# Kernel tuning notes

Hardware: AMD Instinct MI355X
Metric: run time of the kernel (lower is better)

The kernel has to match this reference:

```python
import jax, jax.numpy as jnp
import numpy as np

B, LQ, LK, D = 8, 1024, 4096, 1024


def setup_inputs() -> dict:
    key = jax.random.key(0)
    k1, k2, k3, k4, k5, k6 = jax.random.split(key, 6)
    s = 1.0 / np.sqrt(D)
    return {
        "T": jax.random.normal(k1, (B, LQ, D), dtype=jnp.float32),
        "S": jax.random.normal(k2, (B, LK, D), dtype=jnp.float32),
        "Wq": jax.random.uniform(k3, (D, D), jnp.float32, -s, s),
        "Wk": jax.random.uniform(k4, (D, D), jnp.float32, -s, s),
        "Wv": jax.random.uniform(k5, (D, D), jnp.float32, -s, s),
        "Wo": jax.random.uniform(k6, (D, D), jnp.float32, -s, s),
    }


def reference(T, S, Wq, Wk, Wv, Wo):
    # Linear layers: y = x @ W.T (torch nn.Linear convention), bias=False
    q = jnp.einsum('bqd,ed->bqe', T, Wq)          # [B, LQ, D]
    k = jnp.einsum('bkd,ed->bke', S, Wk)          # [B, LK, D]
    v = jnp.einsum('bkd,ed->bke', S, Wv)          # [B, LK, D]
    scale = jnp.asarray(D, q.dtype) ** -0.5        # hidden_dim ** -0.5 (single head)
    attn = jnp.einsum('bqe,bke->bqk', q, k) * scale  # [B, LQ, LK]
    attn = jax.nn.softmax(attn, axis=-1)
    out = jnp.einsum('bqk,bke->bqe', attn, v)      # [B, LQ, D]
    return jnp.einsum('bqe,fe->bqf', out, Wo)      # output projection
```

## Files before the change

### kernel.cpp

```cpp
#include <hip/hip_runtime.h>
#include <stdint.h>

typedef __bf16 bf16;
typedef __bf16 bf16x8 __attribute__((ext_vector_type(8)));
typedef float f32x4 __attribute__((ext_vector_type(4)));

__device__ __forceinline__ void gload_lds16(const void* g, void* l) {
    __builtin_amdgcn_global_load_lds(
        (const __attribute__((address_space(1))) unsigned int*)g,
        (__attribute__((address_space(3))) unsigned int*)l, 16, 0, 0);
}

#define BAR()    asm volatile("s_barrier" ::: "memory")
#define WAITV(N) asm volatile("s_waitcnt vmcnt(" #N ")" ::: "memory")

template<int OMODE>
__global__ __launch_bounds__(512, 2)
void gemm256(const bf16* __restrict__ A, const bf16* __restrict__ B,
             void* __restrict__ Cv, int K, int N,
             long batchA, long batchB, long batchC, float alpha,
             int nbx, int nby, int GC)
{
    __shared__ __align__(16) bf16 lds[2][4][8192];

    const int nwg  = gridDim.x;
    const int orig = blockIdx.x;
    const int q8   = nwg >> 3, r8 = nwg & 7;
    const int xcd  = orig & 7, lid = orig >> 3;
    const int p    = (xcd < r8 ? xcd * (q8 + 1) : r8 * (q8 + 1) + (xcd - r8) * q8) + lid;
    const int perb = nbx * nby;
    const int z    = p / perb;
    const int pb   = p - z * perb;
    const int sw   = nby * GC;
    const int st   = pb / sw;
    const int rem  = pb - st * sw;
    const int by   = rem / GC;
    const int bx   = st * GC + (rem - by * GC);

    const long rowb = (long)by << 8;
    const long colb = (long)bx << 8;

    const int t  = threadIdx.x;
    const int l  = t & 63;
    const int w  = t >> 6;
    const int wm = w >> 2;
    const int wn = w & 3;

    const int sL   = (t * 16) ^ (((t >> 3) & 3) << 4);
    const int srow = sL >> 6;
    const int sk   = (sL & 63) >> 1;
    const bf16* Ab = A + (long)z * batchA;
    const bf16* Bb = B + (long)z * batchB;
    const bf16* gA = Ab + (rowb + srow) * (long)K + sk;
    const bf16* gB = Bb + (colb + srow) * (long)K + sk;
    const long rstep = 128L * K;
    const int  d0 = t * 8, d1 = t * 8 + 4096;

    const int xl    = ((l >> 1) & 3) << 4;
    const int aBase = ((wm * 128 + (l & 15)) * 64 + ((l >> 4) << 4)) ^ xl;
    const int bBase = ((wn * 64  + (l & 15)) * 64 + ((l >> 4) << 4)) ^ xl;

    f32x4 acc[8][4] = {};
    bf16x8 av[4], bv[4];

#define STG(S, R, G, KOFF) do { \
    const bf16* _g = (G) + (KOFF); \
    gload_lds16(_g,         &lds[S][R][d0]); \
    gload_lds16(_g + rstep, &lds[S][R][d1]); \
  } while (0)

#define RD(S, R, OFF) (*(const bf16x8*)((const char*)&lds[S][R][0] + (OFF)))

#define MM(MB) \
    __builtin_amdgcn_s_setprio(1); \
    _Pragma("unroll") for (int mi = 0; mi < 4; ++mi) \
      _Pragma("unroll") for (int nj = 0; nj < 4; ++nj) \
        acc[MB + mi][nj] = __builtin_amdgcn_mfma_f32_16x16x32_bf16(av[mi], bv[nj], acc[MB + mi][nj], 0, 0, 0); \
    __builtin_amdgcn_s_setprio(0);

#define PH1(S, STGX) { \
    _Pragma("unroll") for (int nj = 0; nj < 4; ++nj) bv[nj] = RD(S, 2, bBase + nj * 1024); \
    _Pragma("unroll") for (int mi = 0; mi < 4; ++mi) av[mi] = RD(S, 0, aBase + mi * 1024); \
    STGX; BAR(); MM(0) BAR(); }

#define PH2(S, STGX) { \
    _Pragma("unroll") for (int mi = 0; mi < 4; ++mi) av[mi] = RD(S, 0, aBase + 4096 + mi * 1024); \
    STGX; BAR(); MM(4) BAR(); }

#define PH3(S, STGX) { \
    _Pragma("unroll") for (int nj = 0; nj < 4; ++nj) bv[nj] = RD(S, 3, bBase + nj * 1024); \
    _Pragma("unroll") for (int mi = 0; mi < 4; ++mi) av[mi] = RD(S, 1, aBase + mi * 1024); \
    STGX; BAR(); MM(0) BAR(); }

#define PH4(S, STGX, WT) { \
    _Pragma("unroll") for (int mi = 0; mi < 4; ++mi) av[mi] = RD(S, 1, aBase + 4096 + mi * 1024); \
    STGX; BAR(); MM(4) WT; BAR(); }

    STG(0, 0, gA, 0);
    STG(0, 1, gA, 32);
    STG(0, 2, gB, 0);
    STG(0, 3, gB, 32);
    STG(1, 2, gB, 64);
    STG(1, 0, gA, 64);
    STG(1, 3, gB, 96);
    WAITV(6);
    BAR();

    const int NI = K >> 7;
    for (int i = 0; i < NI - 1; ++i) {
        const int kb = i << 7;
        const int kn = kb + 128;
        PH1(0, STG(1, 1, gA, kb + 96));
        PH2(0, STG(0, 2, gB, kn));
        PH3(0, STG(0, 0, gA, kn));
        PH4(0, STG(0, 3, gB, kn + 32), WAITV(6));
        PH1(1, STG(0, 1, gA, kn + 32));
        PH2(1, STG(1, 2, gB, kn + 64));
        PH3(1, STG(1, 0, gA, kn + 64));
        PH4(1, STG(1, 3, gB, kn + 96), WAITV(6));
    }
    {
        const int kb = (NI - 1) << 7;
        PH1(0, STG(1, 1, gA, kb + 96));
        PH2(0, );
        PH3(0, );
        PH4(0, , WAITV(0));
        PH1(1, );
        PH2(1, );
        PH3(1, );
        PH4(1, , );
    }
#undef STG
#undef RD
#undef MM
#undef PH1
#undef PH2
#undef PH3
#undef PH4

    const int r0 = (l >> 4) << 2;

    if constexpr (OMODE == 2) {
        const long cb0 = colb + wn * 64 + (l & 15);
        const long rb0 = rowb + wm * 128 + r0;
#pragma unroll
        for (int mf = 0; mf < 8; ++mf)
#pragma unroll
          for (int nj = 0; nj < 4; ++nj) {
            const long col = cb0 + nj * 16;
#pragma unroll
            for (int r = 0; r < 4; ++r) {
                const long row = rb0 + mf * 16 + r;
                ((float*)Cv)[(long)z * batchC + row * (long)N + col] = acc[mf][nj][r] * alpha;
            }
          }
    } else {
        bf16* epi = &lds[0][0][0];
        const int rrow   = t >> 5;
        const int cchunk = (t & 31) << 3;
        const int myh = (OMODE == 0) ? wm : (wn >> 1);
#pragma unroll
        for (int h = 0; h < 2; ++h) {
            if (myh == h) {
#pragma unroll
                for (int mf = 0; mf < 8; ++mf)
#pragma unroll
                  for (int nj = 0; nj < 4; ++nj)
#pragma unroll
                    for (int r = 0; r < 4; ++r) {
                        const float v = acc[mf][nj][r] * alpha;
                        int orow = wm * 128 + mf * 16 + r0 + r;
                        int ocol = wn * 64 + nj * 16 + (l & 15);
                        if (OMODE == 1) { int tmp = orow; orow = ocol; ocol = tmp; }
                        epi[(orow - h * 128) * 280 + ocol] = (bf16)v;
                    }
            }
            __syncthreads();
#pragma unroll
            for (int pp = 0; pp < 8; ++pp) {
                const int lrow = pp * 16 + rrow;
                const int row  = h * 128 + lrow;
                uint4 d = *(const uint4*)&epi[lrow * 280 + cchunk];
                if (OMODE == 0) {
                    bf16* Cb = (bf16*)Cv + (long)z * batchC;
                    *(uint4*)&Cb[(rowb + row) * (long)N + colb + cchunk] = d;
                } else {
                    const long zz  = rowb >> 12;
                    const long lk0 = (rowb & 4095) + cchunk;
                    *(uint4*)&((bf16*)Cv)[zz * 4194304L + (colb + row) * 4096L + lk0] = d;
                }
            }
            __syncthreads();
        }
    }
}

__global__ void cvt_bf16(const float* __restrict__ in, bf16* __restrict__ out, long n8)
{
    const long stride = (long)gridDim.x * 256;
    for (long i = (long)blockIdx.x * 256 + threadIdx.x; i < n8; i += stride) {
        const float4* p = (const float4*)in + i * 2;
        float4 a = p[0], b = p[1];
        union { bf16 h[8]; uint4 u; } o;
        o.h[0] = (bf16)a.x; o.h[1] = (bf16)a.y; o.h[2] = (bf16)a.z; o.h[3] = (bf16)a.w;
        o.h[4] = (bf16)b.x; o.h[5] = (bf16)b.y; o.h[6] = (bf16)b.z; o.h[7] = (bf16)b.w;
        ((uint4*)out)[i] = o.u;
    }
}

__global__ void cvt_w4(const float* __restrict__ wq, const float* __restrict__ wk,
                       const float* __restrict__ wv, const float* __restrict__ wo,
                       bf16* __restrict__ out)
{
    const long i  = (long)blockIdx.x * 256 + threadIdx.x;
    const int seg = (int)(i >> 17);
    const long j  = i & 131071;
    const float* src = seg == 0 ? wq : seg == 1 ? wk : seg == 2 ? wv : wo;
    const float4* pp = (const float4*)src + j * 2;
    float4 a = pp[0], b = pp[1];
    union { bf16 h[8]; uint4 u; } o;
    o.h[0] = (bf16)a.x; o.h[1] = (bf16)a.y; o.h[2] = (bf16)a.z; o.h[3] = (bf16)a.w;
    o.h[4] = (bf16)b.x; o.h[5] = (bf16)b.y; o.h[6] = (bf16)b.z; o.h[7] = (bf16)b.w;
    ((uint4*)out)[i] = o.u;
}

__global__ __launch_bounds__(256)
void softmax_rows(bf16* __restrict__ P)
{
    const long base = (long)blockIdx.x * 4096;
    const int t = threadIdx.x;
    union U { uint4 u; bf16 h[8]; };
    U d0, d1;
    d0.u = *(const uint4*)&P[base + t * 8];
    d1.u = *(const uint4*)&P[base + 2048 + t * 8];
    float v[16];
#pragma unroll
    for (int i = 0; i < 8; ++i) { v[i] = (float)d0.h[i]; v[8 + i] = (float)d1.h[i]; }
    float mx = v[0];
#pragma unroll
    for (int i = 1; i < 16; ++i) mx = fmaxf(mx, v[i]);
    for (int o = 32; o; o >>= 1) mx = fmaxf(mx, __shfl_xor(mx, o));
    __shared__ float redm[4], reds[4];
    if ((t & 63) == 0) redm[t >> 6] = mx;
    __syncthreads();
    mx = fmaxf(fmaxf(redm[0], redm[1]), fmaxf(redm[2], redm[3]));
    float s = 0.f;
#pragma unroll
    for (int i = 0; i < 16; ++i) { v[i] = __expf(v[i] - mx); s += v[i]; }
    for (int o = 32; o; o >>= 1) s += __shfl_xor(s, o);
    if ((t & 63) == 0) reds[t >> 6] = s;
    __syncthreads();
    s = reds[0] + reds[1] + reds[2] + reds[3];
    const float inv = 1.f / s;
    U o0, o1;
#pragma unroll
    for (int i = 0; i < 8; ++i) {
        o0.h[i] = (bf16)(v[i] * inv);
        o1.h[i] = (bf16)(v[8 + i] * inv);
    }
    *(uint4*)&P[base + t * 8]        = o0.u;
    *(uint4*)&P[base + 2048 + t * 8] = o1.u;
}

extern "C" void kernel_launch(void* const* d_in, const int* in_sizes, int n_in,
                              void* d_out, int out_size, void* d_ws, size_t ws_size,
                              hipStream_t stream)
{
    (void)in_sizes; (void)n_in; (void)out_size; (void)ws_size;
    const float* T  = (const float*)d_in[0];
    const float* S  = (const float*)d_in[1];
    const float* Wq = (const float*)d_in[2];
    const float* Wk = (const float*)d_in[3];
    const float* Wv = (const float*)d_in[4];
    const float* Wo = (const float*)d_in[5];
    float* Y = (float*)d_out;
    char* ws = (char*)d_ws;

    bf16* Wqb = (bf16*)(ws + 0);
    bf16* Wkb = (bf16*)(ws + 2097152);
    bf16* Wvb = (bf16*)(ws + 4194304);
    bf16* Wob = (bf16*)(ws + 6291456);
    bf16* Tb  = (bf16*)(ws + 8388608);
    bf16* Ob  = Tb;
    bf16* Qb  = (bf16*)(ws + 25165824);
    bf16* Sb  = (bf16*)(ws + 41943040);
    bf16* Pb  = Sb;
    bf16* Kb  = (bf16*)(ws + 109051904);
    bf16* VTb = (bf16*)(ws + 176160768);

    cvt_w4  <<<2048,  256, 0, stream>>>(Wq, Wk, Wv, Wo, Wqb);
    cvt_bf16<<<4096,  256, 0, stream>>>(T, Tb, 1048576);
    cvt_bf16<<<16384, 256, 0, stream>>>(S, Sb, 4194304);

    gemm256<0><<<128, 512, 0, stream>>>(Tb, Wqb, Qb, 1024, 1024, 0, 0, 0, 1.f, 4, 32, 4);
    gemm256<0><<<512, 512, 0, stream>>>(Sb, Wkb, Kb, 1024, 1024, 0, 0, 0, 1.f, 4, 128, 4);
    gemm256<1><<<512, 512, 0, stream>>>(Sb, Wvb, VTb, 1024, 1024, 0, 0, 0, 1.f, 4, 128, 4);

    gemm256<0><<<512, 512, 0, stream>>>(Qb, Kb, Pb, 1024, 4096,
        1024L * 1024, 4096L * 1024, 1024L * 4096, 0.03125f, 16, 4, 4);

    softmax_rows<<<8192, 256, 0, stream>>>(Pb);

    gemm256<0><<<128, 512, 0, stream>>>(Pb, VTb, Ob, 4096, 1024,
        1024L * 4096, 1024L * 4096, 1024L * 1024, 1.f, 4, 4, 4);

    gemm256<2><<<128, 512, 0, stream>>>(Ob, Wob, Y, 1024, 1024, 0, 0, 0, 1.f, 4, 32, 4);
}
```

Measured before the change: 441.0 us.

## Store all bf16 intermediates in K-panel layout for contiguous GEMM tile loads

```diff
diff --git a/kernel.cpp b/kernel.cpp
--- a/kernel.cpp
+++ b/kernel.cpp
@@ -18,8 +18,9 @@
 __global__ __launch_bounds__(512, 2)
 void gemm256(const bf16* __restrict__ A, const bf16* __restrict__ B,
              void* __restrict__ Cv, int K, int N,
-             long batchA, long batchB, long batchC, float alpha,
-             int nbx, int nby, int GC)
+             long batchA, long batchB, long batchC,
+             long aPanel, long bPanel, long cPanel, long cBatch, int cLog,
+             float alpha, int nbx, int nby, int GC)
 {
     __shared__ __align__(16) bf16 lds[2][4][8192];
 
@@ -46,14 +47,11 @@
     const int wm = w >> 2;
     const int wn = w & 3;
 
-    const int sL   = (t * 16) ^ (((t >> 3) & 3) << 4);
-    const int srow = sL >> 6;
-    const int sk   = (sL & 63) >> 1;
-    const bf16* Ab = A + (long)z * batchA;
-    const bf16* Bb = B + (long)z * batchB;
-    const bf16* gA = Ab + (rowb + srow) * (long)K + sk;
-    const bf16* gB = Bb + (colb + srow) * (long)K + sk;
-    const long rstep = 128L * K;
+    const int sLb = (t * 16) ^ (((t >> 3) & 3) << 4);
+    const char* gAc = (const char*)A + 2L * ((long)z * batchA + rowb * 32);
+    const char* gBc = (const char*)B + 2L * ((long)z * batchB + colb * 32);
+    const long kA = 2L * aPanel;
+    const long kB = 2L * bPanel;
     const int  d0 = t * 8, d1 = t * 8 + 4096;
 
     const int xl    = ((l >> 1) & 3) << 4;
@@ -63,10 +61,10 @@
     f32x4 acc[8][4] = {};
     bf16x8 av[4], bv[4];
 
-#define STG(S, R, G, KOFF) do { \
-    const bf16* _g = (G) + (KOFF); \
-    gload_lds16(_g,         &lds[S][R][d0]); \
-    gload_lds16(_g + rstep, &lds[S][R][d1]); \
+#define STG(S, R, G, KS, P) do { \
+    const char* _g = (G) + (long)(P) * (KS); \
+    gload_lds16(_g + sLb,        &lds[S][R][d0]); \
+    gload_lds16(_g + sLb + 8192, &lds[S][R][d1]); \
   } while (0)
 
 #define RD(S, R, OFF) (*(const bf16x8*)((const char*)&lds[S][R][0] + (OFF)))
@@ -96,32 +94,31 @@
     _Pragma("unroll") for (int mi = 0; mi < 4; ++mi) av[mi] = RD(S, 1, aBase + 4096 + mi * 1024); \
     STGX; BAR(); MM(4) WT; BAR(); }
 
-    STG(0, 0, gA, 0);
-    STG(0, 1, gA, 32);
-    STG(0, 2, gB, 0);
-    STG(0, 3, gB, 32);
-    STG(1, 2, gB, 64);
-    STG(1, 0, gA, 64);
-    STG(1, 3, gB, 96);
+    STG(0, 0, gAc, kA, 0);
+    STG(0, 1, gAc, kA, 1);
+    STG(0, 2, gBc, kB, 0);
+    STG(0, 3, gBc, kB, 1);
+    STG(1, 2, gBc, kB, 2);
+    STG(1, 0, gAc, kA, 2);
+    STG(1, 3, gBc, kB, 3);
     WAITV(6);
     BAR();
 
     const int NI = K >> 7;
     for (int i = 0; i < NI - 1; ++i) {
-        const int kb = i << 7;
-        const int kn = kb + 128;
-        PH1(0, STG(1, 1, gA, kb + 96));
-        PH2(0, STG(0, 2, gB, kn));
-        PH3(0, STG(0, 0, gA, kn));
-        PH4(0, STG(0, 3, gB, kn + 32), WAITV(6));
-        PH1(1, STG(0, 1, gA, kn + 32));
-        PH2(1, STG(1, 2, gB, kn + 64));
-        PH3(1, STG(1, 0, gA, kn + 64));
-        PH4(1, STG(1, 3, gB, kn + 96), WAITV(6));
+        const int pp = i << 2;
+        PH1(0, STG(1, 1, gAc, kA, pp + 3));
+        PH2(0, STG(0, 2, gBc, kB, pp + 4));
+        PH3(0, STG(0, 0, gAc, kA, pp + 4));
+        PH4(0, STG(0, 3, gBc, kB, pp + 5), WAITV(6));
+        PH1(1, STG(0, 1, gAc, kA, pp + 5));
+        PH2(1, STG(1, 2, gBc, kB, pp + 6));
+        PH3(1, STG(1, 0, gAc, kA, pp + 6));
+        PH4(1, STG(1, 3, gBc, kB, pp + 7), WAITV(6));
     }
     {
-        const int kb = (NI - 1) << 7;
-        PH1(0, STG(1, 1, gA, kb + 96));
+        const int pp = (NI - 1) << 2;
+        PH1(0, STG(1, 1, gAc, kA, pp + 3));
         PH2(0, );
         PH3(0, );
         PH4(0, , WAITV(0));
@@ -139,72 +136,66 @@
 #undef PH4
 
     const int r0 = (l >> 4) << 2;
+    const long rbase = rowb + wm * 128 + r0;
+    const long cb0   = colb + wn * 64 + (l & 15);
 
     if constexpr (OMODE == 2) {
-        const long cb0 = colb + wn * 64 + (l & 15);
-        const long rb0 = rowb + wm * 128 + r0;
 #pragma unroll
         for (int mf = 0; mf < 8; ++mf)
 #pragma unroll
           for (int nj = 0; nj < 4; ++nj) {
             const long col = cb0 + nj * 16;
 #pragma unroll
+            for (int r = 0; r < 4; ++r)
+                ((float*)Cv)[(long)z * batchC + (rbase + mf * 16 + r) * (long)N + col]
+                    = acc[mf][nj][r] * alpha;
+          }
+    } else if constexpr (OMODE == 1) {
+#pragma unroll
+        for (int mf = 0; mf < 8; ++mf)
+#pragma unroll
+          for (int nj = 0; nj < 4; ++nj) {
+            const long grow = rbase + mf * 16;
+            const long e    = cb0 + nj * 16;
+            const long zz   = grow >> 12;
+            const long lkz  = grow & 4095;
+            union { bf16 h[4]; uint2 u; } pk;
+#pragma unroll
+            for (int r = 0; r < 4; ++r) pk.h[r] = (bf16)(acc[mf][nj][r] * alpha);
+            *(uint2*)&((bf16*)Cv)[zz * 4194304L + (lkz >> 5) * 32768L + e * 32 + (lkz & 31)] = pk.u;
+          }
+    } else {
+        const long cMask = (1L << cLog) - 1;
+#pragma unroll
+        for (int mf = 0; mf < 8; ++mf)
+#pragma unroll
+          for (int nj = 0; nj < 4; ++nj) {
+            const long gcol = cb0 + nj * 16;
+            const long cpart = (long)z * batchC + (gcol >> 5) * cPanel + (gcol & 31);
+#pragma unroll
             for (int r = 0; r < 4; ++r) {
-                const long row = rb0 + mf * 16 + r;
-                ((float*)Cv)[(long)z * batchC + row * (long)N + col] = acc[mf][nj][r] * alpha;
+                const long grow = rbase + mf * 16 + r;
+                const long idx = cpart + (grow >> cLog) * cBatch + (grow & cMask) * 32;
+                ((bf16*)Cv)[idx] = (bf16)(acc[mf][nj][r] * alpha);
             }
           }
-    } else {
-        bf16* epi = &lds[0][0][0];
-        const int rrow   = t >> 5;
-        const int cchunk = (t & 31) << 3;
-        const int myh = (OMODE == 0) ? wm : (wn >> 1);
-#pragma unroll
-        for (int h = 0; h < 2; ++h) {
-            if (myh == h) {
-#pragma unroll
-                for (int mf = 0; mf < 8; ++mf)
-#pragma unroll
-                  for (int nj = 0; nj < 4; ++nj)
-#pragma unroll
-                    for (int r = 0; r < 4; ++r) {
-                        const float v = acc[mf][nj][r] * alpha;
-                        int orow = wm * 128 + mf * 16 + r0 + r;
-                        int ocol = wn * 64 + nj * 16 + (l & 15);
-                        if (OMODE == 1) { int tmp = orow; orow = ocol; ocol = tmp; }
-                        epi[(orow - h * 128) * 280 + ocol] = (bf16)v;
-                    }
-            }
-            __syncthreads();
-#pragma unroll
-            for (int pp = 0; pp < 8; ++pp) {
-                const int lrow = pp * 16 + rrow;
-                const int row  = h * 128 + lrow;
-                uint4 d = *(const uint4*)&epi[lrow * 280 + cchunk];
-                if (OMODE == 0) {
-                    bf16* Cb = (bf16*)Cv + (long)z * batchC;
-                    *(uint4*)&Cb[(rowb + row) * (long)N + colb + cchunk] = d;
-                } else {
-                    const long zz  = rowb >> 12;
-                    const long lk0 = (rowb & 4095) + cchunk;
-                    *(uint4*)&((bf16*)Cv)[zz * 4194304L + (colb + row) * 4096L + lk0] = d;
-                }
-            }
-            __syncthreads();
-        }
     }
 }
 
-__global__ void cvt_bf16(const float* __restrict__ in, bf16* __restrict__ out, long n8)
+__global__ void cvt_pan(const float* __restrict__ in, bf16* __restrict__ out,
+                        long M, long n8)
 {
     const long stride = (long)gridDim.x * 256;
-    for (long i = (long)blockIdx.x * 256 + threadIdx.x; i < n8; i += stride) {
-        const float4* p = (const float4*)in + i * 2;
-        float4 a = p[0], b = p[1];
+    for (long v = (long)blockIdx.x * 256 + threadIdx.x; v < n8; v += stride) {
+        const float4* pp = (const float4*)in + v * 2;
+        float4 a = pp[0], b = pp[1];
         union { bf16 h[8]; uint4 u; } o;
         o.h[0] = (bf16)a.x; o.h[1] = (bf16)a.y; o.h[2] = (bf16)a.z; o.h[3] = (bf16)a.w;
         o.h[4] = (bf16)b.x; o.h[5] = (bf16)b.y; o.h[6] = (bf16)b.z; o.h[7] = (bf16)b.w;
-        ((uint4*)out)[i] = o.u;
+        const long row = v >> 7;
+        const int  kv  = (int)(v & 127);
+        const long addr = (long)(kv >> 2) * (M * 32) + row * 32 + (kv & 3) * 8;
+        *(uint4*)&out[addr] = o.u;
     }
 }
 
@@ -221,45 +212,62 @@
     union { bf16 h[8]; uint4 u; } o;
     o.h[0] = (bf16)a.x; o.h[1] = (bf16)a.y; o.h[2] = (bf16)a.z; o.h[3] = (bf16)a.w;
     o.h[4] = (bf16)b.x; o.h[5] = (bf16)b.y; o.h[6] = (bf16)b.z; o.h[7] = (bf16)b.w;
-    ((uint4*)out)[i] = o.u;
-}
-
-__global__ __launch_bounds__(256)
-void softmax_rows(bf16* __restrict__ P)
-{
-    const long base = (long)blockIdx.x * 4096;
-    const int t = threadIdx.x;
+    const long row = j >> 7;
+    const int  kv  = (int)(j & 127);
+    out += (long)seg * 1048576;
+    *(uint4*)&out[(long)(kv >> 2) * 32768 + row * 32 + (kv & 3) * 8] = o.u;
+}
+
+__global__ __launch_bounds__(512)
+void softmax_pan(bf16* __restrict__ P)
+{
+    const int t  = threadIdx.x;
+    const int g  = blockIdx.x;
+    const long z = g >> 8;
+    const int r0 = (g & 255) << 2;
+    bf16* rp = P + z * 4194304L + (long)(t >> 2) * 32768L + (long)(r0 + (t & 3)) * 32;
+
     union U { uint4 u; bf16 h[8]; };
-    U d0, d1;
-    d0.u = *(const uint4*)&P[base + t * 8];
-    d1.u = *(const uint4*)&P[base + 2048 + t * 8];
-    float v[16];
-#pragma unroll
-    for (int i = 0; i < 8; ++i) { v[i] = (float)d0.h[i]; v[8 + i] = (float)d1.h[i]; }
+    U d[4];
+#pragma unroll
+    for (int i = 0; i < 4; ++i) d[i].u = ((const uint4*)rp)[i];
+    float v[32];
+#pragma unroll
+    for (int i = 0; i < 32; ++i) v[i] = (float)d[i >> 3].h[i & 7];
+
     float mx = v[0];
 #pragma unroll
-    for (int i = 1; i < 16; ++i) mx = fmaxf(mx, v[i]);
-    for (int o = 32; o; o >>= 1) mx = fmaxf(mx, __shfl_xor(mx, o));
-    __shared__ float redm[4], reds[4];
-    if ((t & 63) == 0) redm[t >> 6] = mx;
+    for (int i = 1; i < 32; ++i) mx = fmaxf(mx, v[i]);
+    mx = fmaxf(mx, __shfl_xor(mx, 4));
+    mx = fmaxf(mx, __shfl_xor(mx, 8));
+    mx = fmaxf(mx, __shfl_xor(mx, 16));
+    mx = fmaxf(mx, __shfl_xor(mx, 32));
+    __shared__ float redm[8][4], reds[8][4];
+    const int wid = t >> 6, l = t & 63;
+    if (l < 4) redm[wid][l] = mx;
     __syncthreads();
-    mx = fmaxf(fmaxf(redm[0], redm[1]), fmaxf(redm[2], redm[3]));
+    mx = redm[0][t & 3];
+#pragma unroll
+    for (int wv2 = 1; wv2 < 8; ++wv2) mx = fmaxf(mx, redm[wv2][t & 3]);
+
     float s = 0.f;
 #pragma unroll
-    for (int i = 0; i < 16; ++i) { v[i] = __expf(v[i] - mx); s += v[i]; }
-    for (int o = 32; o; o >>= 1) s += __shfl_xor(s, o);
-    if ((t & 63) == 0) reds[t >> 6] = s;
+    for (int i = 0; i < 32; ++i) { v[i] = __expf(v[i] - mx); s += v[i]; }
+    s += __shfl_xor(s, 4);
+    s += __shfl_xor(s, 8);
+    s += __shfl_xor(s, 16);
+    s += __shfl_xor(s, 32);
+    if (l < 4) reds[wid][l] = s;
     __syncthreads();
-    s = reds[0] + reds[1] + reds[2] + reds[3];
+    s = 0.f;
+#pragma unroll
+    for (int wv2 = 0; wv2 < 8; ++wv2) s += reds[wv2][t & 3];
+
     const float inv = 1.f / s;
-    U o0, o1;
-#pragma unroll
-    for (int i = 0; i < 8; ++i) {
-        o0.h[i] = (bf16)(v[i] * inv);
-        o1.h[i] = (bf16)(v[8 + i] * inv);
-    }
-    *(uint4*)&P[base + t * 8]        = o0.u;
-    *(uint4*)&P[base + 2048 + t * 8] = o1.u;
+#pragma unroll
+    for (int i = 0; i < 32; ++i) d[i >> 3].h[i & 7] = (bf16)(v[i] * inv);
+#pragma unroll
+    for (int i = 0; i < 4; ++i) ((uint4*)rp)[i] = d[i].u;
 }
 
 extern "C" void kernel_launch(void* const* d_in, const int* in_sizes, int n_in,
@@ -288,21 +296,27 @@
     bf16* Kb  = (bf16*)(ws + 109051904);
     bf16* VTb = (bf16*)(ws + 176160768);
 
-    cvt_w4  <<<2048,  256, 0, stream>>>(Wq, Wk, Wv, Wo, Wqb);
-    cvt_bf16<<<4096,  256, 0, stream>>>(T, Tb, 1048576);
-    cvt_bf16<<<16384, 256, 0, stream>>>(S, Sb, 4194304);
-
-    gemm256<0><<<128, 512, 0, stream>>>(Tb, Wqb, Qb, 1024, 1024, 0, 0, 0, 1.f, 4, 32, 4);
-    gemm256<0><<<512, 512, 0, stream>>>(Sb, Wkb, Kb, 1024, 1024, 0, 0, 0, 1.f, 4, 128, 4);
-    gemm256<1><<<512, 512, 0, stream>>>(Sb, Wvb, VTb, 1024, 1024, 0, 0, 0, 1.f, 4, 128, 4);
+    cvt_w4 <<<2048,  256, 0, stream>>>(Wq, Wk, Wv, Wo, Wqb);
+    cvt_pan<<<4096,  256, 0, stream>>>(T, Tb, 8192,  1048576);
+    cvt_pan<<<16384, 256, 0, stream>>>(S, Sb, 32768, 4194304);
+
+    gemm256<0><<<128, 512, 0, stream>>>(Tb, Wqb, Qb, 1024, 1024,
+        0, 0, 0, 262144, 32768, 32768, 1048576, 10, 1.f, 4, 32, 4);
+    gemm256<0><<<512, 512, 0, stream>>>(Sb, Wkb, Kb, 1024, 1024,
+        0, 0, 0, 1048576, 32768, 131072, 4194304, 12, 1.f, 4, 128, 4);
+    gemm256<1><<<512, 512, 0, stream>>>(Sb, Wvb, VTb, 1024, 1024,
+        0, 0, 0, 1048576, 32768, 0, 0, 30, 1.f, 4, 128, 4);
 
     gemm256<0><<<512, 512, 0, stream>>>(Qb, Kb, Pb, 1024, 4096,
-        1024L * 1024, 4096L * 1024, 1024L * 4096, 0.03125f, 16, 4, 4);
-
-    softmax_rows<<<8192, 256, 0, stream>>>(Pb);
+        1048576, 4194304, 4194304, 32768, 131072, 32768, 0, 30,
+        0.03125f, 16, 4, 4);
+
+    softmax_pan<<<2048, 512, 0, stream>>>(Pb);
 
     gemm256<0><<<128, 512, 0, stream>>>(Pb, VTb, Ob, 4096, 1024,
-        1024L * 4096, 1024L * 4096, 1024L * 1024, 1.f, 4, 4, 4);
-
-    gemm256<2><<<128, 512, 0, stream>>>(Ob, Wob, Y, 1024, 1024, 0, 0, 0, 1.f, 4, 32, 4);
-}
+        4194304, 4194304, 1048576, 32768, 32768, 32768, 0, 30,
+        1.f, 4, 4, 4);
+
+    gemm256<2><<<128, 512, 0, stream>>>(Ob, Wob, Y, 1024, 1024,
+        1048576, 0, 1048576, 32768, 32768, 0, 0, 30, 1.f, 4, 4, 4);
+}
```

Result: slower. 452.6 us (+2.6%).

## Split-K the P·V GEMM into two halves with fp32 partials and reduce

Applied to the files above, without the earlier changes.

```diff
diff --git a/kernel.cpp b/kernel.cpp
--- a/kernel.cpp
+++ b/kernel.cpp
@@ -19,7 +19,7 @@
 void gemm256(const bf16* __restrict__ A, const bf16* __restrict__ B,
              void* __restrict__ Cv, int K, int N,
              long batchA, long batchB, long batchC, float alpha,
-             int nbx, int nby, int GC)
+             int nbx, int nby, int GC, int lda, int ldb)
 {
     __shared__ __align__(16) bf16 lds[2][4][8192];
 
@@ -28,9 +28,14 @@
     const int q8   = nwg >> 3, r8 = nwg & 7;
     const int xcd  = orig & 7, lid = orig >> 3;
     const int p    = (xcd < r8 ? xcd * (q8 + 1) : r8 * (q8 + 1) + (xcd - r8) * q8) + lid;
+
+    int pd = p, hv = 0;
+    if constexpr (OMODE == 3) { hv = p >> 7; pd = p & 127; }
+    const int kOff = hv << 11;
+
     const int perb = nbx * nby;
-    const int z    = p / perb;
-    const int pb   = p - z * perb;
+    const int z    = pd / perb;
+    const int pb   = pd - z * perb;
     const int sw   = nby * GC;
     const int st   = pb / sw;
     const int rem  = pb - st * sw;
@@ -49,11 +54,10 @@
     const int sL   = (t * 16) ^ (((t >> 3) & 3) << 4);
     const int srow = sL >> 6;
     const int sk   = (sL & 63) >> 1;
-    const bf16* Ab = A + (long)z * batchA;
-    const bf16* Bb = B + (long)z * batchB;
-    const bf16* gA = Ab + (rowb + srow) * (long)K + sk;
-    const bf16* gB = Bb + (colb + srow) * (long)K + sk;
-    const long rstep = 128L * K;
+    const bf16* gA = A + (long)z * batchA + (rowb + srow) * (long)lda + sk + kOff;
+    const bf16* gB = B + (long)z * batchB + (colb + srow) * (long)ldb + sk + kOff;
+    const long rA = 128L * lda;
+    const long rB = 128L * ldb;
     const int  d0 = t * 8, d1 = t * 8 + 4096;
 
     const int xl    = ((l >> 1) & 3) << 4;
@@ -63,10 +67,10 @@
     f32x4 acc[8][4] = {};
     bf16x8 av[4], bv[4];
 
-#define STG(S, R, G, KOFF) do { \
-    const bf16* _g = (G) + (KOFF); \
-    gload_lds16(_g,         &lds[S][R][d0]); \
-    gload_lds16(_g + rstep, &lds[S][R][d1]); \
+#define STG(S, R, G, KOFF2, RS) do { \
+    const bf16* _g = (G) + (KOFF2); \
+    gload_lds16(_g,      &lds[S][R][d0]); \
+    gload_lds16(_g + RS, &lds[S][R][d1]); \
   } while (0)
 
 #define RD(S, R, OFF) (*(const bf16x8*)((const char*)&lds[S][R][0] + (OFF)))
@@ -96,13 +100,13 @@
     _Pragma("unroll") for (int mi = 0; mi < 4; ++mi) av[mi] = RD(S, 1, aBase + 4096 + mi * 1024); \
     STGX; BAR(); MM(4) WT; BAR(); }
 
-    STG(0, 0, gA, 0);
-    STG(0, 1, gA, 32);
-    STG(0, 2, gB, 0);
-    STG(0, 3, gB, 32);
-    STG(1, 2, gB, 64);
-    STG(1, 0, gA, 64);
-    STG(1, 3, gB, 96);
+    STG(0, 0, gA, 0,  rA);
+    STG(0, 1, gA, 32, rA);
+    STG(0, 2, gB, 0,  rB);
+    STG(0, 3, gB, 32, rB);
+    STG(1, 2, gB, 64, rB);
+    STG(1, 0, gA, 64, rA);
+    STG(1, 3, gB, 96, rB);
     WAITV(6);
     BAR();
 
@@ -110,18 +114,18 @@
     for (int i = 0; i < NI - 1; ++i) {
         const int kb = i << 7;
         const int kn = kb + 128;
-        PH1(0, STG(1, 1, gA, kb + 96));
-        PH2(0, STG(0, 2, gB, kn));
-        PH3(0, STG(0, 0, gA, kn));
-        PH4(0, STG(0, 3, gB, kn + 32), WAITV(6));
-        PH1(1, STG(0, 1, gA, kn + 32));
-        PH2(1, STG(1, 2, gB, kn + 64));
-        PH3(1, STG(1, 0, gA, kn + 64));
-        PH4(1, STG(1, 3, gB, kn + 96), WAITV(6));
+        PH1(0, STG(1, 1, gA, kb + 96, rA));
+        PH2(0, STG(0, 2, gB, kn,      rB));
+        PH3(0, STG(0, 0, gA, kn,      rA));
+        PH4(0, STG(0, 3, gB, kn + 32, rB), WAITV(6));
+        PH1(1, STG(0, 1, gA, kn + 32, rA));
+        PH2(1, STG(1, 2, gB, kn + 64, rB));
+        PH3(1, STG(1, 0, gA, kn + 64, rA));
+        PH4(1, STG(1, 3, gB, kn + 96, rB), WAITV(6));
     }
     {
         const int kb = (NI - 1) << 7;
-        PH1(0, STG(1, 1, gA, kb + 96));
+        PH1(0, STG(1, 1, gA, kb + 96, rA));
         PH2(0, );
         PH3(0, );
         PH4(0, , WAITV(0));
@@ -153,6 +157,19 @@
                 const long row = rb0 + mf * 16 + r;
                 ((float*)Cv)[(long)z * batchC + row * (long)N + col] = acc[mf][nj][r] * alpha;
             }
+          }
+    } else if constexpr (OMODE == 3) {
+        float* Cb = (float*)Cv + (long)hv * 8388608 + (long)z * 1048576;
+        const long cb0 = colb + wn * 64 + (l & 15);
+        const long rb0 = rowb + wm * 128 + r0;
+#pragma unroll
+        for (int mf = 0; mf < 8; ++mf)
+#pragma unroll
+          for (int nj = 0; nj < 4; ++nj) {
+            const long col = cb0 + nj * 16;
+#pragma unroll
+            for (int r = 0; r < 4; ++r)
+                Cb[(rb0 + mf * 16 + r) * 1024 + col] = acc[mf][nj][r];
           }
     } else {
         bf16* epi = &lds[0][0][0];
@@ -224,6 +241,20 @@
     ((uint4*)out)[i] = o.u;
 }
 
+__global__ void reduce_pv(const float* __restrict__ Pt, bf16* __restrict__ Ob)
+{
+    const long i = (long)blockIdx.x * 256 + threadIdx.x;
+    const float4* a = (const float4*)Pt + i * 2;
+    const float4* b = (const float4*)(Pt + 8388608) + i * 2;
+    float4 x0 = a[0], x1 = a[1], y0 = b[0], y1 = b[1];
+    union { bf16 h[8]; uint4 u; } o;
+    o.h[0] = (bf16)(x0.x + y0.x); o.h[1] = (bf16)(x0.y + y0.y);
+    o.h[2] = (bf16)(x0.z + y0.z); o.h[3] = (bf16)(x0.w + y0.w);
+    o.h[4] = (bf16)(x1.x + y1.x); o.h[5] = (bf16)(x1.y + y1.y);
+    o.h[6] = (bf16)(x1.z + y1.z); o.h[7] = (bf16)(x1.w + y1.w);
+    ((uint4*)Ob)[i] = o.u;
+}
+
 __global__ __launch_bounds__(256)
 void softmax_rows(bf16* __restrict__ P)
 {
@@ -286,23 +317,29 @@
     bf16* Sb  = (bf16*)(ws + 41943040);
     bf16* Pb  = Sb;
     bf16* Kb  = (bf16*)(ws + 109051904);
+    float* Pt = (float*)Kb;
     bf16* VTb = (bf16*)(ws + 176160768);
 
     cvt_w4  <<<2048,  256, 0, stream>>>(Wq, Wk, Wv, Wo, Wqb);
     cvt_bf16<<<4096,  256, 0, stream>>>(T, Tb, 1048576);
     cvt_bf16<<<16384, 256, 0, stream>>>(S, Sb, 4194304);
 
-    gemm256<0><<<128, 512, 0, stream>>>(Tb, Wqb, Qb, 1024, 1024, 0, 0, 0, 1.f, 4, 32, 4);
-    gemm256<0><<<512, 512, 0, stream>>>(Sb, Wkb, Kb, 1024, 1024, 0, 0, 0, 1.f, 4, 128, 4);
-    gemm256<1><<<512, 512, 0, stream>>>(Sb, Wvb, VTb, 1024, 1024, 0, 0, 0, 1.f, 4, 128, 4);
+    gemm256<0><<<128, 512, 0, stream>>>(Tb, Wqb, Qb, 1024, 1024,
+        0, 0, 0, 1.f, 4, 32, 4, 1024, 1024);
+    gemm256<0><<<512, 512, 0, stream>>>(Sb, Wkb, Kb, 1024, 1024,
+        0, 0, 0, 1.f, 4, 128, 4, 1024, 1024);
+    gemm256<1><<<512, 512, 0, stream>>>(Sb, Wvb, VTb, 1024, 1024,
+        0, 0, 0, 1.f, 4, 128, 4, 1024, 1024);
 
     gemm256<0><<<512, 512, 0, stream>>>(Qb, Kb, Pb, 1024, 4096,
-        1024L * 1024, 4096L * 1024, 1024L * 4096, 0.03125f, 16, 4, 4);
+        1024L * 1024, 4096L * 1024, 1024L * 4096, 0.03125f, 16, 4, 4, 1024, 1024);
 
     softmax_rows<<<8192, 256, 0, stream>>>(Pb);
 
-    gemm256<0><<<128, 512, 0, stream>>>(Pb, VTb, Ob, 4096, 1024,
-        1024L * 4096, 1024L * 4096, 1024L * 1024, 1.f, 4, 4, 4);
-
-    gemm256<2><<<128, 512, 0, stream>>>(Ob, Wob, Y, 1024, 1024, 0, 0, 0, 1.f, 4, 32, 4);
-}
+    gemm256<3><<<256, 512, 0, stream>>>(Pb, VTb, Pt, 2048, 1024,
+        1024L * 4096, 1024L * 4096, 1048576, 1.f, 4, 4, 4, 4096, 4096);
+    reduce_pv<<<4096, 256, 0, stream>>>(Pt, Ob);
+
+    gemm256<2><<<128, 512, 0, stream>>>(Ob, Wob, Y, 1024, 1024,
+        0, 0, 0, 1.f, 4, 32, 4, 1024, 1024);
+}
```

Measured after the change: 425.5 us. 3.5% less time.
